# Kernel optimization log

Hardware: AMD Instinct MI355X
Metric: run time of the kernel (lower is better)

The kernel has to match this reference:

```python
import jax, jax.numpy as jnp
import numpy as np

N = 50000      # nodes
E = 800000     # edges (avg degree 16)
IN = 128       # in_channels
OUT = 64       # out_channels (latent)
H = 2 * OUT    # hidden = 2*out_channels


def setup_inputs() -> dict:
    key = jax.random.key(0)
    ks = jax.random.split(key, 7)
    s = 0.1
    return {
        "x": jax.random.normal(ks[0], (N, IN), jnp.float32),
        "edge_index": jax.random.randint(ks[1], (2, E), 0, N, dtype=jnp.int64),
        "W1": jax.random.normal(ks[2], (IN, H), jnp.float32) * s,
        "b1": jnp.zeros((H,), jnp.float32),
        "Wmu": jax.random.normal(ks[3], (H, OUT), jnp.float32) * s,
        "bmu": jnp.zeros((OUT,), jnp.float32),
        "Wls": jax.random.normal(ks[4], (H, OUT), jnp.float32) * s,
        "bls": jnp.zeros((OUT,), jnp.float32),
        "eps": jax.random.normal(ks[5], (N, OUT), jnp.float32),
    }


def _gcn_conv(x, W, b, src, dst, dinv):
    # GCNConv: h = W x, out = D^-1/2 (A + I) D^-1/2 h + b
    h = x @ W                                   # [N, F]
    norm = (dinv[src] * dinv[dst])[:, None]     # [E, 1]
    agg = jax.ops.segment_sum(h[src] * norm, dst, num_segments=N)
    agg = agg + h * (dinv * dinv)[:, None]      # self-loop term
    return agg + b


def reference(x, edge_index, W1, b1, Wmu, bmu, Wls, bls, eps):
    src, dst = edge_index[0], edge_index[1]
    # degree with self-loops (PyG gcn_norm counts in-degree on dst/col)
    deg = jax.ops.segment_sum(jnp.ones((E,), x.dtype), dst, num_segments=N) + 1.0
    dinv = deg ** -0.5  # deg >= 1, safe

    h = jax.nn.relu(_gcn_conv(x, W1, b1, src, dst, dinv))
    mu = _gcn_conv(h, Wmu, bmu, src, dst, dinv)
    # Faithful to source bug: logstd also uses convmu weights
    logstd = _gcn_conv(h, Wmu, bmu, src, dst, dinv)
    # training-mode reparameterization with externally supplied noise
    zeta = mu + eps * jnp.exp(logstd)
    return (mu, logstd, zeta)
```

## Files before the change

kernel.cpp:

```cpp
#include <hip/hip_runtime.h>
#include <math.h>

#define N_NODES 50000
#define N_EDGES 800000
#define IN_C    128
#define H_C     128
#define OUT_C   64
#define BCAP    64
#define EPB     2048
#define CSTRIDE 16

typedef unsigned char  u8;
typedef unsigned short u16;
typedef unsigned int   u32;

__device__ __forceinline__ u16 f2bf(float f) {
    u32 u; __builtin_memcpy(&u, &f, 4);
    u += 0x7FFFu + ((u >> 16) & 1u);
    return (u16)(u >> 16);
}
__device__ __forceinline__ float bflo(u32 p) { u32 u = p << 16;         float f; __builtin_memcpy(&f, &u, 4); return f; }
__device__ __forceinline__ float bfhi(u32 p) { u32 u = p & 0xFFFF0000u; float f; __builtin_memcpy(&f, &u, 4); return f; }

__global__ void k_zero(float4* __restrict__ p, int n4) {
    int i = blockIdx.x * 256 + threadIdx.x;
    if (i < n4) p[i] = make_float4(0.f, 0.f, 0.f, 0.f);
}

__global__ void k_detect_i64(const int* __restrict__ ei, int* __restrict__ flag) {
    int t = threadIdx.x;
    int nz = 0;
    for (int i = t; i < 256; i += 64)
        if (ei[2 * i + 1] != 0) nz = 1;
    unsigned long long b = __ballot(nz != 0);
    if (t == 0) *flag = (b == 0ULL) ? 1 : 0;
}

__device__ __forceinline__ int eidx(const int* __restrict__ ei, size_t pos, int mode) {
    return mode ? ei[pos << 1] : ei[pos];
}

__global__ void k_wcvt(const float* __restrict__ W, u16* __restrict__ Wbf) {
    int i = blockIdx.x * 256 + threadIdx.x;
    if (i < IN_C * H_C) Wbf[i] = f2bf(W[i]);
}

__global__ void k_compact(const int* __restrict__ ei, const int* __restrict__ flag,
                          u16* __restrict__ src16, u16* __restrict__ dst16) {
    int e = blockIdx.x * 256 + threadIdx.x;
    if (e >= N_EDGES) return;
    int m = *flag;
    src16[e] = (u16)eidx(ei, (size_t)e, m);
    dst16[e] = (u16)eidx(ei, (size_t)N_EDGES + e, m);
}

__global__ void k_sort(const u16* __restrict__ dst16, const u16* __restrict__ src16,
                       int* __restrict__ cursor, u16* __restrict__ sorted_src) {
    const int part = blockIdx.x & 7;
    const int base = (blockIdx.x >> 3) * EPB;
    for (int i = threadIdx.x; i < EPB; i += 256) {
        int e = base + i;
        if (e >= N_EDGES) break;
        int d = dst16[e];
        if ((d & 7) != part) continue;
        int c = atomicAdd(&cursor[(size_t)d << 4], 1);
        if (c < BCAP) sorted_src[((size_t)d << 6) + c] = src16[e];
    }
}

__global__ void k_dinv(const int* __restrict__ cursor, float* __restrict__ dinv,
                       u8* __restrict__ cnt8) {
    int i = blockIdx.x * blockDim.x + threadIdx.x;
    if (i < N_NODES) {
        int c = cursor[(size_t)i << 4];
        dinv[i] = rsqrtf((float)c + 1.0f);
        cnt8[i] = (u8)(c > BCAP ? BCAP : c);
    }
}

__launch_bounds__(512, 4)
__global__ void k_gemm1(const float* __restrict__ X, const u16* __restrict__ Wbf,
                        const float* __restrict__ dinv, u16* __restrict__ outq) {
    __shared__ __align__(16) char lds[65536];
    const int tid = threadIdx.x, wv = tid >> 6, lane = tid & 63;
    const int row0 = blockIdx.x * 64 + wv * 8;
    const size_t limit = (size_t)N_NODES * 512 - 1024;
    const char* Xb = (const char*)X;
    const char* Wb = (const char*)Wbf;

#pragma unroll
    for (int chk = 0; chk < 4; ++chk) {
        size_t off = (size_t)row0 * 512 + (size_t)chk * 1024;
        if (off > limit) off = limit;
        __builtin_amdgcn_global_load_lds(
            (const __attribute__((address_space(1))) void*)(Xb + off + (size_t)lane * 16),
            (__attribute__((address_space(3))) void*)(lds + wv * 4096 + chk * 1024),
            16, 0, 0);
    }
#pragma unroll
    for (int chk = 0; chk < 4; ++chk) {
        int wc = wv * 4 + chk;
        __builtin_amdgcn_global_load_lds(
            (const __attribute__((address_space(1))) void*)(Wb + (size_t)wc * 1024 + (size_t)lane * 16),
            (__attribute__((address_space(3))) void*)(lds + 32768 + wc * 1024),
            16, 0, 0);
    }
    asm volatile("s_waitcnt vmcnt(0)" ::: "memory");
    __syncthreads();

    const int c4 = (lane & 31) * 4;
    const int rs = lane >> 5;

    float4 acc[4];
#pragma unroll
    for (int r = 0; r < 4; ++r) acc[r] = make_float4(0.f, 0.f, 0.f, 0.f);

#pragma unroll 2
    for (int k4 = 0; k4 < IN_C / 4; ++k4) {
        float4 xv[4];
#pragma unroll
        for (int r = 0; r < 4; ++r)
            xv[r] = *reinterpret_cast<const float4*>(
                &lds[wv * 4096 + (rs + r * 2) * 512 + k4 * 16]);
        float4 w[4];
#pragma unroll
        for (int r = 0; r < 4; ++r) {
            uint2 wu = *reinterpret_cast<const uint2*>(
                &lds[32768 + (4 * k4 + r) * 256 + (lane & 31) * 8]);
            w[r].x = bflo(wu.x); w[r].y = bfhi(wu.x);
            w[r].z = bflo(wu.y); w[r].w = bfhi(wu.y);
        }
#pragma unroll
        for (int r = 0; r < 4; ++r) {
            acc[r].x = fmaf(xv[r].x, w[0].x, acc[r].x);
            acc[r].y = fmaf(xv[r].x, w[0].y, acc[r].y);
            acc[r].z = fmaf(xv[r].x, w[0].z, acc[r].z);
            acc[r].w = fmaf(xv[r].x, w[0].w, acc[r].w);
            acc[r].x = fmaf(xv[r].y, w[1].x, acc[r].x);
            acc[r].y = fmaf(xv[r].y, w[1].y, acc[r].y);
            acc[r].z = fmaf(xv[r].y, w[1].z, acc[r].z);
            acc[r].w = fmaf(xv[r].y, w[1].w, acc[r].w);
            acc[r].x = fmaf(xv[r].z, w[2].x, acc[r].x);
            acc[r].y = fmaf(xv[r].z, w[2].y, acc[r].y);
            acc[r].z = fmaf(xv[r].z, w[2].z, acc[r].z);
            acc[r].w = fmaf(xv[r].z, w[2].w, acc[r].w);
            acc[r].x = fmaf(xv[r].w, w[3].x, acc[r].x);
            acc[r].y = fmaf(xv[r].w, w[3].y, acc[r].y);
            acc[r].z = fmaf(xv[r].w, w[3].z, acc[r].z);
            acc[r].w = fmaf(xv[r].w, w[3].w, acc[r].w);
        }
    }

#pragma unroll
    for (int r = 0; r < 4; ++r) {
        int row = row0 + rs + r * 2;
        if (row < N_NODES) {
            float di = dinv[row];
            ushort4 o;
            o.x = f2bf(acc[r].x * di);
            o.y = f2bf(acc[r].y * di);
            o.z = f2bf(acc[r].z * di);
            o.w = f2bf(acc[r].w * di);
            *reinterpret_cast<ushort4*>(outq + (size_t)row * H_C + c4) = o;
        }
    }
}

__launch_bounds__(256, 4)
__global__ void k_gemm2(const u16* __restrict__ gbuf, const float* __restrict__ W,
                        u16* __restrict__ outp) {
    __shared__ __align__(16) char xs[32768];
    const int tid = threadIdx.x, wv = tid >> 6, lane = tid & 63;
    const int row0 = blockIdx.x * 128 + wv * 32;
    const size_t limit = (size_t)N_NODES * 256 - 1024;
    const char* Gb = (const char*)gbuf;

#pragma unroll
    for (int chk = 0; chk < 8; ++chk) {
        size_t off = (size_t)row0 * 256 + (size_t)chk * 1024;
        if (off > limit) off = limit;
        __builtin_amdgcn_global_load_lds(
            (const __attribute__((address_space(1))) void*)(Gb + off + (size_t)lane * 16),
            (__attribute__((address_space(3))) void*)(xs + wv * 8192 + chk * 1024),
            16, 0, 0);
    }
    asm volatile("s_waitcnt vmcnt(0)" ::: "memory");
    __builtin_amdgcn_sched_barrier(0);

    const int c4 = (lane & 15) * 4;
    const int rs = lane >> 4;

    float4 acc[8];
#pragma unroll
    for (int r = 0; r < 8; ++r) acc[r] = make_float4(0.f, 0.f, 0.f, 0.f);

#pragma unroll 2
    for (int k4 = 0; k4 < IN_C / 4; ++k4) {
        float4 xv[8];
#pragma unroll
        for (int r = 0; r < 8; ++r) {
            int rl = rs + r * 4;
            uint2 u = *reinterpret_cast<const uint2*>(
                &xs[wv * 8192 + rl * 256 + k4 * 8]);
            xv[r].x = bflo(u.x); xv[r].y = bfhi(u.x);
            xv[r].z = bflo(u.y); xv[r].w = bfhi(u.y);
        }
        float4 w0 = *reinterpret_cast<const float4*>(W + (size_t)(4 * k4 + 0) * OUT_C + c4);
        float4 w1 = *reinterpret_cast<const float4*>(W + (size_t)(4 * k4 + 1) * OUT_C + c4);
        float4 w2 = *reinterpret_cast<const float4*>(W + (size_t)(4 * k4 + 2) * OUT_C + c4);
        float4 w3 = *reinterpret_cast<const float4*>(W + (size_t)(4 * k4 + 3) * OUT_C + c4);
#pragma unroll
        for (int r = 0; r < 8; ++r) {
            acc[r].x = fmaf(xv[r].x, w0.x, acc[r].x);
            acc[r].y = fmaf(xv[r].x, w0.y, acc[r].y);
            acc[r].z = fmaf(xv[r].x, w0.z, acc[r].z);
            acc[r].w = fmaf(xv[r].x, w0.w, acc[r].w);
            acc[r].x = fmaf(xv[r].y, w1.x, acc[r].x);
            acc[r].y = fmaf(xv[r].y, w1.y, acc[r].y);
            acc[r].z = fmaf(xv[r].y, w1.z, acc[r].z);
            acc[r].w = fmaf(xv[r].y, w1.w, acc[r].w);
            acc[r].x = fmaf(xv[r].z, w2.x, acc[r].x);
            acc[r].y = fmaf(xv[r].z, w2.y, acc[r].y);
            acc[r].z = fmaf(xv[r].z, w2.z, acc[r].z);
            acc[r].w = fmaf(xv[r].z, w2.w, acc[r].w);
            acc[r].x = fmaf(xv[r].w, w3.x, acc[r].x);
            acc[r].y = fmaf(xv[r].w, w3.y, acc[r].y);
            acc[r].z = fmaf(xv[r].w, w3.z, acc[r].z);
            acc[r].w = fmaf(xv[r].w, w3.w, acc[r].w);
        }
    }

#pragma unroll
    for (int r = 0; r < 8; ++r) {
        int row = row0 + rs + r * 4;
        if (row < N_NODES) {
            ushort4 o;
            o.x = f2bf(acc[r].x);
            o.y = f2bf(acc[r].y);
            o.z = f2bf(acc[r].z);
            o.w = f2bf(acc[r].w);
            *reinterpret_cast<ushort4*>(outp + (size_t)row * OUT_C + c4) = o;
        }
    }
}

template <int C, int MODE>
__global__ void k_agg(const u16* __restrict__ sorted_src,
                      const u8* __restrict__ cnt8,
                      const float* __restrict__ dinv,
                      const u16* __restrict__ rows,
                      const float* __restrict__ bias,
                      const float* __restrict__ eps,
                      void* __restrict__ outbuf) {
    const int wave = threadIdx.x >> 6;
    const int lane = threadIdx.x & 63;
    const int n = blockIdx.x * 4 + wave;
    if (n >= N_NODES) return;

    const int c = cnt8[n];
    const int beg = n << 6;
    const int end = beg + c;
    const float di = dinv[n];

    if (C == 128) {
        const u32* rw = reinterpret_cast<const u32*>(rows);
        const int pi = lane;
        float a0 = 0.f, a1 = 0.f, b0 = 0.f, b1 = 0.f;
        int j = beg;
        for (; j + 8 <= end; j += 8) {
            ushort4 sa = *reinterpret_cast<const ushort4*>(sorted_src + j);
            ushort4 sb = *reinterpret_cast<const ushort4*>(sorted_src + j + 4);
            u32 p0 = rw[(size_t)sa.x * 64 + pi];
            u32 p1 = rw[(size_t)sa.y * 64 + pi];
            u32 p2 = rw[(size_t)sa.z * 64 + pi];
            u32 p3 = rw[(size_t)sa.w * 64 + pi];
            u32 p4 = rw[(size_t)sb.x * 64 + pi];
            u32 p5 = rw[(size_t)sb.y * 64 + pi];
            u32 p6 = rw[(size_t)sb.z * 64 + pi];
            u32 p7 = rw[(size_t)sb.w * 64 + pi];
            a0 += bflo(p0) + bflo(p2);  a1 += bfhi(p0) + bfhi(p2);
            b0 += bflo(p1) + bflo(p3);  b1 += bfhi(p1) + bfhi(p3);
            a0 += bflo(p4) + bflo(p6);  a1 += bfhi(p4) + bfhi(p6);
            b0 += bflo(p5) + bflo(p7);  b1 += bfhi(p5) + bfhi(p7);
        }
        for (; j + 4 <= end; j += 4) {
            ushort4 sa = *reinterpret_cast<const ushort4*>(sorted_src + j);
            u32 p0 = rw[(size_t)sa.x * 64 + pi];
            u32 p1 = rw[(size_t)sa.y * 64 + pi];
            u32 p2 = rw[(size_t)sa.z * 64 + pi];
            u32 p3 = rw[(size_t)sa.w * 64 + pi];
            a0 += bflo(p0) + bflo(p2);  a1 += bfhi(p0) + bfhi(p2);
            b0 += bflo(p1) + bflo(p3);  b1 += bfhi(p1) + bfhi(p3);
        }
        for (; j < end; ++j) {
            u32 p0 = rw[(size_t)sorted_src[j] * 64 + pi];
            a0 += bflo(p0); a1 += bfhi(p0);
        }
        u32 qn = rw[(size_t)n * 64 + pi];
        const int c0 = lane * 2;
        float px = fmaf(di, a0 + b0 + bflo(qn), bias[c0]);
        float py = fmaf(di, a1 + b1 + bfhi(qn), bias[c0 + 1]);
        ushort2 o;
        o.x = f2bf(di * fmaxf(px, 0.f));
        o.y = f2bf(di * fmaxf(py, 0.f));
        *reinterpret_cast<ushort2*>((u16*)outbuf + (size_t)n * 128 + c0) = o;
    } else {
        float a0 = 0.f, a1 = 0.f, b0 = 0.f, b1 = 0.f;
        int j = beg;
        for (; j + 8 <= end; j += 8) {
            ushort4 sa = *reinterpret_cast<const ushort4*>(sorted_src + j);
            ushort4 sb = *reinterpret_cast<const ushort4*>(sorted_src + j + 4);
            float f0, f1, f2, f3, f4, f5, f6, f7;
            { u32 u = (u32)rows[(size_t)sa.x * 64 + lane] << 16; __builtin_memcpy(&f0, &u, 4); }
            { u32 u = (u32)rows[(size_t)sa.y * 64 + lane] << 16; __builtin_memcpy(&f1, &u, 4); }
            { u32 u = (u32)rows[(size_t)sa.z * 64 + lane] << 16; __builtin_memcpy(&f2, &u, 4); }
            { u32 u = (u32)rows[(size_t)sa.w * 64 + lane] << 16; __builtin_memcpy(&f3, &u, 4); }
            { u32 u = (u32)rows[(size_t)sb.x * 64 + lane] << 16; __builtin_memcpy(&f4, &u, 4); }
            { u32 u = (u32)rows[(size_t)sb.y * 64 + lane] << 16; __builtin_memcpy(&f5, &u, 4); }
            { u32 u = (u32)rows[(size_t)sb.z * 64 + lane] << 16; __builtin_memcpy(&f6, &u, 4); }
            { u32 u = (u32)rows[(size_t)sb.w * 64 + lane] << 16; __builtin_memcpy(&f7, &u, 4); }
            a0 += f0 + f2;  a1 += f1 + f3;
            b0 += f4 + f6;  b1 += f5 + f7;
        }
        for (; j + 4 <= end; j += 4) {
            ushort4 sa = *reinterpret_cast<const ushort4*>(sorted_src + j);
            float f0, f1, f2, f3;
            { u32 u = (u32)rows[(size_t)sa.x * 64 + lane] << 16; __builtin_memcpy(&f0, &u, 4); }
            { u32 u = (u32)rows[(size_t)sa.y * 64 + lane] << 16; __builtin_memcpy(&f1, &u, 4); }
            { u32 u = (u32)rows[(size_t)sa.z * 64 + lane] << 16; __builtin_memcpy(&f2, &u, 4); }
            { u32 u = (u32)rows[(size_t)sa.w * 64 + lane] << 16; __builtin_memcpy(&f3, &u, 4); }
            a0 += f0 + f2;  a1 += f1 + f3;
        }
        for (; j < end; ++j) {
            u32 u = (u32)rows[(size_t)sorted_src[j] * 64 + lane] << 16;
            float f; __builtin_memcpy(&f, &u, 4);
            a0 += f;
        }
        float pn;
        { u32 u = (u32)rows[(size_t)n * 64 + lane] << 16; __builtin_memcpy(&pn, &u, 4); }
        float* out = (float*)outbuf;
        float m = fmaf(di, (a0 + a1) + (b0 + b1) + pn, bias[lane]);
        const int NM = N_NODES * OUT_C;
        int i = n * 64 + lane;
        float z = fmaf(eps[i], expf(m), m);
        out[i]          = m;
        out[NM + i]     = m;
        out[2 * NM + i] = z;
    }
}

extern "C" void kernel_launch(void* const* d_in, const int* in_sizes, int n_in,
                              void* d_out, int out_size, void* d_ws, size_t ws_size,
                              hipStream_t stream) {
    const float* x   = (const float*)d_in[0];
    const int*   ei  = (const int*)d_in[1];
    const float* W1  = (const float*)d_in[2];
    const float* b1  = (const float*)d_in[3];
    const float* Wmu = (const float*)d_in[4];
    const float* bmu = (const float*)d_in[5];
    const float* eps = (const float*)d_in[8];
    float* out = (float*)d_out;

    char* p = (char*)d_ws;
    int*  flag   = (int*)p;                        p += 16;
    int*  cursor = (int*)p;                        p += (size_t)N_NODES * CSTRIDE * 4;
    float* dinv  = (float*)p;                      p += ((size_t)N_NODES * 4 + 15) / 16 * 16;
    u8*  cnt8    = (u8*)p;                         p += ((size_t)N_NODES + 15) / 16 * 16;
    u16* wbf     = (u16*)p;                        p += (size_t)IN_C * H_C * 2;
    u16* sorted  = (u16*)p;                        p += ((size_t)N_NODES * BCAP * 2 + 15) / 16 * 16;
    u16* bufA    = (u16*)p;                        p += ((size_t)N_NODES * H_C * 2 + 15) / 16 * 16;
    u16* bufG    = (u16*)p;
    u16* bufP    = bufA;
    u16* src16   = bufG;
    u16* dst16   = bufG + (size_t)N_EDGES;

    k_zero<<<(N_NODES * CSTRIDE / 4 + 255) / 256, 256, 0, stream>>>(
        (float4*)cursor, N_NODES * CSTRIDE / 4);
    k_detect_i64<<<1, 64, 0, stream>>>(ei, flag);
    k_wcvt<<<(IN_C * H_C + 255) / 256, 256, 0, stream>>>(W1, wbf);
    k_compact<<<(N_EDGES + 255) / 256, 256, 0, stream>>>(ei, flag, src16, dst16);
    k_sort<<<8 * ((N_EDGES + EPB - 1) / EPB), 256, 0, stream>>>(dst16, src16, cursor, sorted);
    k_dinv<<<(N_NODES + 255) / 256, 256, 0, stream>>>(cursor, dinv, cnt8);

    k_gemm1<<<(N_NODES + 63) / 64, 512, 0, stream>>>(x, wbf, dinv, bufA);
    k_agg<H_C, 0><<<(N_NODES + 3) / 4, 256, 0, stream>>>(sorted, cnt8, dinv, bufA, b1, nullptr, bufG);
    k_gemm2<<<(N_NODES + 127) / 128, 256, 0, stream>>>(bufG, Wmu, bufP);
    k_agg<OUT_C, 1><<<(N_NODES + 3) / 4, 256, 0, stream>>>(sorted, cnt8, dinv, bufP, bmu, eps, out);
}
```

Measured before the change: 181.9 us.

## Process two nodes per wave in aggregation and fuse preprocessing kernels

The aggregation kernels now assign each node to a half-wave of 32 lanes, so one wave handles two nodes. Each lane loads wider vectors (uint2 for 128 channels, u32 for 64) and writes vectorized outputs, which halves the number of wavefronts and raises bytes per load. The cursor zeroing, weight conversion and edge compaction kernels are merged into one launch to cut launch overhead. The risk is more divergence between the two nodes in a wave, since their degrees differ, and higher register use per lane.

```diff
diff --git a/kernel.cpp b/kernel.cpp
--- a/kernel.cpp
+++ b/kernel.cpp
@@ -22,11 +22,6 @@
 __device__ __forceinline__ float bflo(u32 p) { u32 u = p << 16;         float f; __builtin_memcpy(&f, &u, 4); return f; }
 __device__ __forceinline__ float bfhi(u32 p) { u32 u = p & 0xFFFF0000u; float f; __builtin_memcpy(&f, &u, 4); return f; }
 
-__global__ void k_zero(float4* __restrict__ p, int n4) {
-    int i = blockIdx.x * 256 + threadIdx.x;
-    if (i < n4) p[i] = make_float4(0.f, 0.f, 0.f, 0.f);
-}
-
 __global__ void k_detect_i64(const int* __restrict__ ei, int* __restrict__ flag) {
     int t = threadIdx.x;
     int nz = 0;
@@ -40,18 +35,18 @@
     return mode ? ei[pos << 1] : ei[pos];
 }
 
-__global__ void k_wcvt(const float* __restrict__ W, u16* __restrict__ Wbf) {
+__global__ void k_pre(const int* __restrict__ ei, const int* __restrict__ flag,
+                      const float* __restrict__ W, u16* __restrict__ Wbf,
+                      int4* __restrict__ cursor4,
+                      u16* __restrict__ src16, u16* __restrict__ dst16) {
     int i = blockIdx.x * 256 + threadIdx.x;
+    if (i < N_NODES * CSTRIDE / 4) cursor4[i] = make_int4(0, 0, 0, 0);
     if (i < IN_C * H_C) Wbf[i] = f2bf(W[i]);
-}
-
-__global__ void k_compact(const int* __restrict__ ei, const int* __restrict__ flag,
-                          u16* __restrict__ src16, u16* __restrict__ dst16) {
-    int e = blockIdx.x * 256 + threadIdx.x;
-    if (e >= N_EDGES) return;
-    int m = *flag;
-    src16[e] = (u16)eidx(ei, (size_t)e, m);
-    dst16[e] = (u16)eidx(ei, (size_t)N_EDGES + e, m);
+    if (i < N_EDGES) {
+        int m = *flag;
+        src16[i] = (u16)eidx(ei, (size_t)i, m);
+        dst16[i] = (u16)eidx(ei, (size_t)N_EDGES + i, m);
+    }
 }
 
 __global__ void k_sort(const u16* __restrict__ dst16, const u16* __restrict__ src16,
@@ -253,99 +248,113 @@
                       const float* __restrict__ eps,
                       void* __restrict__ outbuf) {
     const int wave = threadIdx.x >> 6;
-    const int lane = threadIdx.x & 63;
-    const int n = blockIdx.x * 4 + wave;
+    const int half = (threadIdx.x >> 5) & 1;
+    const int hl   = threadIdx.x & 31;
+    const int n = blockIdx.x * 8 + wave * 2 + half;
     if (n >= N_NODES) return;
 
     const int c = cnt8[n];
-    const int beg = n << 6;
-    const int end = beg + c;
+    const u16* bk = sorted_src + ((size_t)n << 6);
     const float di = dinv[n];
 
     if (C == 128) {
+        const uint2* rw = reinterpret_cast<const uint2*>(rows);
+        float a0 = 0.f, a1 = 0.f, a2 = 0.f, a3 = 0.f;
+        float b0 = 0.f, b1 = 0.f, b2 = 0.f, b3 = 0.f;
+        int j = 0;
+        for (; j + 8 <= c; j += 8) {
+            ushort4 sa = *reinterpret_cast<const ushort4*>(bk + j);
+            ushort4 sb = *reinterpret_cast<const ushort4*>(bk + j + 4);
+            uint2 p0 = rw[(size_t)sa.x * 32 + hl];
+            uint2 p1 = rw[(size_t)sa.y * 32 + hl];
+            uint2 p2 = rw[(size_t)sa.z * 32 + hl];
+            uint2 p3 = rw[(size_t)sa.w * 32 + hl];
+            uint2 p4 = rw[(size_t)sb.x * 32 + hl];
+            uint2 p5 = rw[(size_t)sb.y * 32 + hl];
+            uint2 p6 = rw[(size_t)sb.z * 32 + hl];
+            uint2 p7 = rw[(size_t)sb.w * 32 + hl];
+            a0 += bflo(p0.x) + bflo(p2.x);  a1 += bfhi(p0.x) + bfhi(p2.x);
+            a2 += bflo(p0.y) + bflo(p2.y);  a3 += bfhi(p0.y) + bfhi(p2.y);
+            b0 += bflo(p1.x) + bflo(p3.x);  b1 += bfhi(p1.x) + bfhi(p3.x);
+            b2 += bflo(p1.y) + bflo(p3.y);  b3 += bfhi(p1.y) + bfhi(p3.y);
+            a0 += bflo(p4.x) + bflo(p6.x);  a1 += bfhi(p4.x) + bfhi(p6.x);
+            a2 += bflo(p4.y) + bflo(p6.y);  a3 += bfhi(p4.y) + bfhi(p6.y);
+            b0 += bflo(p5.x) + bflo(p7.x);  b1 += bfhi(p5.x) + bfhi(p7.x);
+            b2 += bflo(p5.y) + bflo(p7.y);  b3 += bfhi(p5.y) + bfhi(p7.y);
+        }
+        for (; j + 4 <= c; j += 4) {
+            ushort4 sa = *reinterpret_cast<const ushort4*>(bk + j);
+            uint2 p0 = rw[(size_t)sa.x * 32 + hl];
+            uint2 p1 = rw[(size_t)sa.y * 32 + hl];
+            uint2 p2 = rw[(size_t)sa.z * 32 + hl];
+            uint2 p3 = rw[(size_t)sa.w * 32 + hl];
+            a0 += bflo(p0.x) + bflo(p2.x);  a1 += bfhi(p0.x) + bfhi(p2.x);
+            a2 += bflo(p0.y) + bflo(p2.y);  a3 += bfhi(p0.y) + bfhi(p2.y);
+            b0 += bflo(p1.x) + bflo(p3.x);  b1 += bfhi(p1.x) + bfhi(p3.x);
+            b2 += bflo(p1.y) + bflo(p3.y);  b3 += bfhi(p1.y) + bfhi(p3.y);
+        }
+        for (; j < c; ++j) {
+            uint2 p = rw[(size_t)bk[j] * 32 + hl];
+            a0 += bflo(p.x); a1 += bfhi(p.x);
+            a2 += bflo(p.y); a3 += bfhi(p.y);
+        }
+        uint2 qn = rw[(size_t)n * 32 + hl];
+        const int c0 = hl * 4;
+        float4 bs = *reinterpret_cast<const float4*>(bias + c0);
+        float q0 = fmaf(di, a0 + b0 + bflo(qn.x), bs.x);
+        float q1 = fmaf(di, a1 + b1 + bfhi(qn.x), bs.y);
+        float q2 = fmaf(di, a2 + b2 + bflo(qn.y), bs.z);
+        float q3 = fmaf(di, a3 + b3 + bfhi(qn.y), bs.w);
+        uint2 o;
+        o.x = (u32)f2bf(di * fmaxf(q0, 0.f)) | ((u32)f2bf(di * fmaxf(q1, 0.f)) << 16);
+        o.y = (u32)f2bf(di * fmaxf(q2, 0.f)) | ((u32)f2bf(di * fmaxf(q3, 0.f)) << 16);
+        reinterpret_cast<uint2*>(outbuf)[(size_t)n * 32 + hl] = o;
+    } else {
         const u32* rw = reinterpret_cast<const u32*>(rows);
-        const int pi = lane;
         float a0 = 0.f, a1 = 0.f, b0 = 0.f, b1 = 0.f;
-        int j = beg;
-        for (; j + 8 <= end; j += 8) {
-            ushort4 sa = *reinterpret_cast<const ushort4*>(sorted_src + j);
-            ushort4 sb = *reinterpret_cast<const ushort4*>(sorted_src + j + 4);
-            u32 p0 = rw[(size_t)sa.x * 64 + pi];
-            u32 p1 = rw[(size_t)sa.y * 64 + pi];
-            u32 p2 = rw[(size_t)sa.z * 64 + pi];
-            u32 p3 = rw[(size_t)sa.w * 64 + pi];
-            u32 p4 = rw[(size_t)sb.x * 64 + pi];
-            u32 p5 = rw[(size_t)sb.y * 64 + pi];
-            u32 p6 = rw[(size_t)sb.z * 64 + pi];
-            u32 p7 = rw[(size_t)sb.w * 64 + pi];
+        int j = 0;
+        for (; j + 8 <= c; j += 8) {
+            ushort4 sa = *reinterpret_cast<const ushort4*>(bk + j);
+            ushort4 sb = *reinterpret_cast<const ushort4*>(bk + j + 4);
+            u32 p0 = rw[(size_t)sa.x * 32 + hl];
+            u32 p1 = rw[(size_t)sa.y * 32 + hl];
+            u32 p2 = rw[(size_t)sa.z * 32 + hl];
+            u32 p3 = rw[(size_t)sa.w * 32 + hl];
+            u32 p4 = rw[(size_t)sb.x * 32 + hl];
+            u32 p5 = rw[(size_t)sb.y * 32 + hl];
+            u32 p6 = rw[(size_t)sb.z * 32 + hl];
+            u32 p7 = rw[(size_t)sb.w * 32 + hl];
             a0 += bflo(p0) + bflo(p2);  a1 += bfhi(p0) + bfhi(p2);
             b0 += bflo(p1) + bflo(p3);  b1 += bfhi(p1) + bfhi(p3);
             a0 += bflo(p4) + bflo(p6);  a1 += bfhi(p4) + bfhi(p6);
             b0 += bflo(p5) + bflo(p7);  b1 += bfhi(p5) + bfhi(p7);
         }
-        for (; j + 4 <= end; j += 4) {
-            ushort4 sa = *reinterpret_cast<const ushort4*>(sorted_src + j);
-            u32 p0 = rw[(size_t)sa.x * 64 + pi];
-            u32 p1 = rw[(size_t)sa.y * 64 + pi];
-            u32 p2 = rw[(size_t)sa.z * 64 + pi];
-            u32 p3 = rw[(size_t)sa.w * 64 + pi];
+        for (; j + 4 <= c; j += 4) {
+            ushort4 sa = *reinterpret_cast<const ushort4*>(bk + j);
+            u32 p0 = rw[(size_t)sa.x * 32 + hl];
+            u32 p1 = rw[(size_t)sa.y * 32 + hl];
+            u32 p2 = rw[(size_t)sa.z * 32 + hl];
+            u32 p3 = rw[(size_t)sa.w * 32 + hl];
             a0 += bflo(p0) + bflo(p2);  a1 += bfhi(p0) + bfhi(p2);
             b0 += bflo(p1) + bflo(p3);  b1 += bfhi(p1) + bfhi(p3);
         }
-        for (; j < end; ++j) {
-            u32 p0 = rw[(size_t)sorted_src[j] * 64 + pi];
-            a0 += bflo(p0); a1 += bfhi(p0);
-        }
-        u32 qn = rw[(size_t)n * 64 + pi];
-        const int c0 = lane * 2;
-        float px = fmaf(di, a0 + b0 + bflo(qn), bias[c0]);
-        float py = fmaf(di, a1 + b1 + bfhi(qn), bias[c0 + 1]);
-        ushort2 o;
-        o.x = f2bf(di * fmaxf(px, 0.f));
-        o.y = f2bf(di * fmaxf(py, 0.f));
-        *reinterpret_cast<ushort2*>((u16*)outbuf + (size_t)n * 128 + c0) = o;
-    } else {
-        float a0 = 0.f, a1 = 0.f, b0 = 0.f, b1 = 0.f;
-        int j = beg;
-        for (; j + 8 <= end; j += 8) {
-            ushort4 sa = *reinterpret_cast<const ushort4*>(sorted_src + j);
-            ushort4 sb = *reinterpret_cast<const ushort4*>(sorted_src + j + 4);
-            float f0, f1, f2, f3, f4, f5, f6, f7;
-            { u32 u = (u32)rows[(size_t)sa.x * 64 + lane] << 16; __builtin_memcpy(&f0, &u, 4); }
-            { u32 u = (u32)rows[(size_t)sa.y * 64 + lane] << 16; __builtin_memcpy(&f1, &u, 4); }
-            { u32 u = (u32)rows[(size_t)sa.z * 64 + lane] << 16; __builtin_memcpy(&f2, &u, 4); }
-            { u32 u = (u32)rows[(size_t)sa.w * 64 + lane] << 16; __builtin_memcpy(&f3, &u, 4); }
-            { u32 u = (u32)rows[(size_t)sb.x * 64 + lane] << 16; __builtin_memcpy(&f4, &u, 4); }
-            { u32 u = (u32)rows[(size_t)sb.y * 64 + lane] << 16; __builtin_memcpy(&f5, &u, 4); }
-            { u32 u = (u32)rows[(size_t)sb.z * 64 + lane] << 16; __builtin_memcpy(&f6, &u, 4); }
-            { u32 u = (u32)rows[(size_t)sb.w * 64 + lane] << 16; __builtin_memcpy(&f7, &u, 4); }
-            a0 += f0 + f2;  a1 += f1 + f3;
-            b0 += f4 + f6;  b1 += f5 + f7;
-        }
-        for (; j + 4 <= end; j += 4) {
-            ushort4 sa = *reinterpret_cast<const ushort4*>(sorted_src + j);
-            float f0, f1, f2, f3;
-            { u32 u = (u32)rows[(size_t)sa.x * 64 + lane] << 16; __builtin_memcpy(&f0, &u, 4); }
-            { u32 u = (u32)rows[(size_t)sa.y * 64 + lane] << 16; __builtin_memcpy(&f1, &u, 4); }
-            { u32 u = (u32)rows[(size_t)sa.z * 64 + lane] << 16; __builtin_memcpy(&f2, &u, 4); }
-            { u32 u = (u32)rows[(size_t)sa.w * 64 + lane] << 16; __builtin_memcpy(&f3, &u, 4); }
-            a0 += f0 + f2;  a1 += f1 + f3;
-        }
-        for (; j < end; ++j) {
-            u32 u = (u32)rows[(size_t)sorted_src[j] * 64 + lane] << 16;
-            float f; __builtin_memcpy(&f, &u, 4);
-            a0 += f;
-        }
-        float pn;
-        { u32 u = (u32)rows[(size_t)n * 64 + lane] << 16; __builtin_memcpy(&pn, &u, 4); }
-        float* out = (float*)outbuf;
-        float m = fmaf(di, (a0 + a1) + (b0 + b1) + pn, bias[lane]);
+        for (; j < c; ++j) {
+            u32 p = rw[(size_t)bk[j] * 32 + hl];
+            a0 += bflo(p); a1 += bfhi(p);
+        }
+        u32 pn = rw[(size_t)n * 32 + hl];
+        const int ch = hl * 2;
+        float m0 = fmaf(di, (a0 + b0) + bflo(pn), bias[ch]);
+        float m1 = fmaf(di, (a1 + b1) + bfhi(pn), bias[ch + 1]);
         const int NM = N_NODES * OUT_C;
-        int i = n * 64 + lane;
-        float z = fmaf(eps[i], expf(m), m);
-        out[i]          = m;
-        out[NM + i]     = m;
-        out[2 * NM + i] = z;
+        int i = n * 64 + ch;
+        float2 e = *reinterpret_cast<const float2*>(eps + i);
+        float z0 = fmaf(e.x, expf(m0), m0);
+        float z1 = fmaf(e.y, expf(m1), m1);
+        float* o = (float*)outbuf;
+        *reinterpret_cast<float2*>(o + i)          = make_float2(m0, m1);
+        *reinterpret_cast<float2*>(o + NM + i)     = make_float2(m0, m1);
+        *reinterpret_cast<float2*>(o + 2 * NM + i) = make_float2(z0, z1);
     }
 }
 
@@ -374,16 +383,14 @@
     u16* src16   = bufG;
     u16* dst16   = bufG + (size_t)N_EDGES;
 
-    k_zero<<<(N_NODES * CSTRIDE / 4 + 255) / 256, 256, 0, stream>>>(
-        (float4*)cursor, N_NODES * CSTRIDE / 4);
     k_detect_i64<<<1, 64, 0, stream>>>(ei, flag);
-    k_wcvt<<<(IN_C * H_C + 255) / 256, 256, 0, stream>>>(W1, wbf);
-    k_compact<<<(N_EDGES + 255) / 256, 256, 0, stream>>>(ei, flag, src16, dst16);
+    k_pre<<<(N_EDGES + 255) / 256, 256, 0, stream>>>(ei, flag, W1, wbf,
+                                                     (int4*)cursor, src16, dst16);
     k_sort<<<8 * ((N_EDGES + EPB - 1) / EPB), 256, 0, stream>>>(dst16, src16, cursor, sorted);
     k_dinv<<<(N_NODES + 255) / 256, 256, 0, stream>>>(cursor, dinv, cnt8);
 
     k_gemm1<<<(N_NODES + 63) / 64, 512, 0, stream>>>(x, wbf, dinv, bufA);
-    k_agg<H_C, 0><<<(N_NODES + 3) / 4, 256, 0, stream>>>(sorted, cnt8, dinv, bufA, b1, nullptr, bufG);
+    k_agg<H_C, 0><<<(N_NODES + 7) / 8, 256, 0, stream>>>(sorted, cnt8, dinv, bufA, b1, nullptr, bufG);
     k_gemm2<<<(N_NODES + 127) / 128, 256, 0, stream>>>(bufG, Wmu, bufP);
-    k_agg<OUT_C, 1><<<(N_NODES + 3) / 4, 256, 0, stream>>>(sorted, cnt8, dinv, bufP, bmu, eps, out);
-}
+    k_agg<OUT_C, 1><<<(N_NODES + 7) / 8, 256, 0, stream>>>(sorted, cnt8, dinv, bufP, bmu, eps, out);
+}
```

Measured after the change: 173.4 us. 1.05x faster.
